# Kernel optimization log

Hardware: AMD Instinct MI355X
Metric: run time of the kernel (lower is better)

The kernel has to match this reference:

```python
import jax, jax.numpy as jnp
import numpy as np

IN_F = 256
OUT_F = 256
ALPHA = 0.01  # LeakyReLU negative slope
NEG_INF = -1e9


def setup_inputs() -> dict:
    key = jax.random.key(0)
    k_inp, k_adj, k_W, k_a = jax.random.split(key, 4)
    inp = jax.random.normal(k_inp, (8, 2048, IN_F), dtype=jnp.float32)
    adj = jax.random.randint(k_adj, (2048, 2048), 0, 2, dtype=jnp.int32)
    # xavier_uniform with gain=1.414
    gain = 1.414
    lim_W = gain * np.sqrt(6.0 / (IN_F + OUT_F))
    W = jax.random.uniform(k_W, (IN_F, OUT_F), minval=-lim_W, maxval=lim_W, dtype=jnp.float32)
    lim_a = gain * np.sqrt(6.0 / (2 * OUT_F + 1))
    a = jax.random.uniform(k_a, (2 * OUT_F, 1), minval=-lim_a, maxval=lim_a, dtype=jnp.float32)
    return {"inp": inp, "adj": adj, "W": W, "a": a}


def reference(inp, adj, W, a):
    # h: [B, N, F]
    h = jnp.matmul(inp, W)
    # Additive attention decomposed: e_ij = leaky_relu(h_i . a1 + h_j . a2)
    # (mathematically identical to concat([h_i, h_j]) @ a, without the O(N^2 * 2F) intermediate)
    a1 = a[:OUT_F, 0]  # [F]
    a2 = a[OUT_F:, 0]  # [F]
    e_src = jnp.einsum('bnf,f->bn', h, a1)  # [B, N]
    e_dst = jnp.einsum('bnf,f->bn', h, a2)  # [B, N]
    e = jax.nn.leaky_relu(e_src[:, :, None] + e_dst[:, None, :], negative_slope=ALPHA)  # [B, N, N]
    e = jnp.where(adj[None, :, :] == 0, NEG_INF, e)
    attention = jax.nn.softmax(e, axis=-1)
    # dropout is identity in eval mode
    h_prime = jnp.matmul(attention, h)  # [B, N, F]
    return jax.nn.relu(h_prime)  # concat=True path
```

## Files before the change

### kernel.cpp

```cpp
#include <hip/hip_runtime.h>
#include <hip/hip_bf16.h>
#include <stdint.h>

#define N_NODES 2048
#define FDIM 256

typedef short bf16x8 __attribute__((ext_vector_type(8)));
typedef float f32x4 __attribute__((ext_vector_type(4)));
typedef unsigned short u16x4 __attribute__((ext_vector_type(4)));

static __device__ __forceinline__ unsigned short bf16r(float x) {
  __hip_bfloat16 h = __float2bfloat16(x);
  return __builtin_bit_cast(unsigned short, h);
}

__global__ __launch_bounds__(256) void k_pp(const int* __restrict__ adj, uint32_t* __restrict__ adjp,
                                            const float* __restrict__ W, const float* __restrict__ a,
                                            __hip_bfloat16* __restrict__ WT16,
                                            float* __restrict__ wa1, float* __restrict__ wa2) {
  int bid = blockIdx.x, t = threadIdx.x;
  if (bid < 512) {
    int lane = t & 63;
    int i = bid * 4 + (t >> 6);
    const int* row = adj + (size_t)i * N_NODES;
    #pragma unroll
    for (int it = 0; it < 32; ++it) {
      int v = row[it * 64 + lane];
      unsigned long long m = __ballot(v != 0);
      if (lane == 0) {
        adjp[i * 64 + it * 2]     = (uint32_t)(m & 0xffffffffull);
        adjp[i * 64 + it * 2 + 1] = (uint32_t)(m >> 32);
      }
    }
    return;
  }
  int pb = bid - 512;
  if (pb < 16) {
    __shared__ __hip_bfloat16 T[64][67];
    int k0 = (pb & 3) * 64, f0 = (pb >> 2) * 64;
    int r = t >> 2, c0 = (t & 3) * 16;
    #pragma unroll
    for (int i = 0; i < 4; ++i) {
      f32x4 v = *(const f32x4*)(W + (size_t)(k0 + r) * FDIM + f0 + c0 + i * 4);
      #pragma unroll
      for (int j = 0; j < 4; ++j) T[r][c0 + i * 4 + j] = __float2bfloat16(v[j]);
    }
    __syncthreads();
    int fr = t >> 2, kc = (t & 3) * 16;
    unsigned short buf[16];
    #pragma unroll
    for (int i = 0; i < 16; ++i) buf[i] = __builtin_bit_cast(unsigned short, T[kc + i][fr]);
    uint4* dst = (uint4*)(WT16 + (size_t)(f0 + fr) * FDIM + k0 + kc);
    dst[0] = *(uint4*)&buf[0];
    dst[1] = *(uint4*)&buf[8];
  } else {
    int k = (pb - 16) * 64 + (t >> 2), q = t & 3;
    float s1 = 0.f, s2 = 0.f;
    #pragma unroll
    for (int i = 0; i < 16; ++i) {
      int f = q * 64 + i * 4;
      f32x4 w  = *(const f32x4*)(W + (size_t)k * FDIM + f);
      f32x4 v1 = *(const f32x4*)(a + f);
      f32x4 v2 = *(const f32x4*)(a + FDIM + f);
      #pragma unroll
      for (int j = 0; j < 4; ++j) { s1 += w[j] * v1[j]; s2 += w[j] * v2[j]; }
    }
    s1 += __shfl_xor(s1, 1); s1 += __shfl_xor(s1, 2);
    s2 += __shfl_xor(s2, 1); s2 += __shfl_xor(s2, 2);
    if (q == 0) { wa1[k] = s1; wa2[k] = s2; }
  }
}

__global__ __launch_bounds__(256) void k_h2(const float* __restrict__ inp,
                                            const __hip_bfloat16* __restrict__ WT16,
                                            const float* __restrict__ wa1, const float* __restrict__ wa2,
                                            __hip_bfloat16* __restrict__ Bf,
                                            float* __restrict__ e_src, float* __restrict__ e_dst) {
  __shared__ char lds_raw[20480];
  __hip_bfloat16* Asm = (__hip_bfloat16*)lds_raw;
  int t = threadIdx.x;
  int r0 = blockIdx.x * 32;
  int b = r0 >> 11, j0 = r0 & (N_NODES - 1);
  {
    int r = t >> 3, q = t & 7, c0 = q * 32;
    const float* ip = inp + (size_t)(r0 + r) * FDIM + c0;
    float s1 = 0.f, s2 = 0.f;
    #pragma unroll
    for (int i = 0; i < 8; ++i) {
      f32x4 v  = *(const f32x4*)(ip + i * 4);
      f32x4 u1 = *(const f32x4*)(wa1 + c0 + i * 4);
      f32x4 u2 = *(const f32x4*)(wa2 + c0 + i * 4);
      u16x4 pk;
      #pragma unroll
      for (int j = 0; j < 4; ++j) {
        s1 += v[j] * u1[j];
        s2 += v[j] * u2[j];
        pk[j] = bf16r(v[j]);
      }
      *(u16x4*)(Asm + r * 264 + c0 + i * 4) = pk;
    }
    s1 += __shfl_xor(s1, 1); s1 += __shfl_xor(s1, 2); s1 += __shfl_xor(s1, 4);
    s2 += __shfl_xor(s2, 1); s2 += __shfl_xor(s2, 2); s2 += __shfl_xor(s2, 4);
    if (q == 0) { e_src[r0 + r] = s1; e_dst[r0 + r] = s2; }
  }
  __syncthreads();

  int lane = t & 63, wv = t >> 6, l15 = lane & 15, lq = lane >> 4;
  int f0 = wv * 64;
  f32x4 acc[2][4];
  #pragma unroll
  for (int mf = 0; mf < 2; ++mf)
    #pragma unroll
    for (int nf = 0; nf < 4; ++nf)
      #pragma unroll
      for (int e = 0; e < 4; ++e) acc[mf][nf][e] = 0.f;

  #pragma unroll
  for (int ks = 0; ks < 8; ++ks) {
    int k0 = ks * 32;
    bf16x8 af[2], bfr[4];
    #pragma unroll
    for (int mf = 0; mf < 2; ++mf)
      af[mf] = *(const bf16x8*)(Asm + (mf * 16 + l15) * 264 + k0 + lq * 8);
    #pragma unroll
    for (int nf = 0; nf < 4; ++nf)
      bfr[nf] = *(const bf16x8*)(WT16 + (size_t)(f0 + nf * 16 + l15) * FDIM + k0 + lq * 8);
    #pragma unroll
    for (int mf = 0; mf < 2; ++mf)
      #pragma unroll
      for (int nf = 0; nf < 4; ++nf)
        acc[mf][nf] = __builtin_amdgcn_mfma_f32_16x16x32_bf16(af[mf], bfr[nf], acc[mf][nf], 0, 0, 0);
  }

  __syncthreads();
  __hip_bfloat16* Tsm = (__hip_bfloat16*)lds_raw;
  #pragma unroll
  for (int mf = 0; mf < 2; ++mf)
    #pragma unroll
    for (int nf = 0; nf < 4; ++nf) {
      u16x4 pk;
      #pragma unroll
      for (int r = 0; r < 4; ++r) pk[r] = bf16r(acc[mf][nf][r]);
      int fl = f0 + nf * 16 + l15;
      int jl = mf * 16 + lq * 4;
      *(u16x4*)(Tsm + fl * 40 + jl) = pk;
    }
  __syncthreads();
  {
    int kt = j0 >> 5;
    #pragma unroll
    for (int q = 0; q < 4; ++q) {
      int ft = (t >> 6) * 4 + q;
      uint4 v = *(const uint4*)(Tsm + (ft * 16 + l15) * 40 + lq * 8);
      *(uint4*)(Bf + ((((size_t)b * 16 + ft) * 64 + kt) * 64 + lane) * 8) = v;
    }
  }
}

__global__ __launch_bounds__(256) void k_ml(const uint32_t* __restrict__ adjp,
                                            const float* __restrict__ e_src,
                                            const float* __restrict__ e_dst,
                                            float* __restrict__ mrow, float* __restrict__ ilrow) {
  int t = threadIdx.x;
  int lane = t & 63;
  int r = blockIdx.x * 4 + (t >> 6);
  int b = r >> 11, i = r & (N_NODES - 1);
  float es = e_src[r];
  const float* edb = e_dst + ((size_t)b << 11);
  const uint32_t* arow = adjp + (size_t)i * 64;
  float ev[32];
  float mx = -3e38f;
  #pragma unroll
  for (int it = 0; it < 32; ++it) {
    int j = it * 64 + lane;
    float ed = edb[j];
    uint32_t w = arow[j >> 5];
    float s = es + ed;
    float lr = fmaxf(s, 0.01f * s);
    float e = ((w >> (j & 31)) & 1u) ? lr : -1e9f;
    ev[it] = e;
    mx = fmaxf(mx, e);
  }
  #pragma unroll
  for (int m = 1; m <= 32; m <<= 1) mx = fmaxf(mx, __shfl_xor(mx, m));
  float sum = 0.f;
  #pragma unroll
  for (int it = 0; it < 32; ++it) sum += __expf(ev[it] - mx);
  #pragma unroll
  for (int m = 1; m <= 32; m <<= 1) sum += __shfl_xor(sum, m);
  if (lane == 0) { mrow[r] = mx; ilrow[r] = 1.0f / sum; }
}

__global__ __launch_bounds__(512) void k_pvF3(const __hip_bfloat16* __restrict__ Bf,
                                              const uint32_t* __restrict__ adjp,
                                              const float* __restrict__ e_src,
                                              const float* __restrict__ e_dst,
                                              const float* __restrict__ mrow,
                                              const float* __restrict__ ilrow,
                                              float* __restrict__ out) {
  __shared__ __align__(16) char Abuf[32768];
  __shared__ float sm_ed[2048];
  __shared__ uint32_t sm_adj[64 * 65];
  int t = threadIdx.x;
  int b  = blockIdx.x & 7;
  int it = blockIdx.x >> 3;
  int i0 = it * 64;
  int lane = t & 63, wv = t >> 6, l15 = lane & 15, lq = lane >> 4;
  int sub = wv & 3, par = wv >> 2;

  *(f32x4*)(sm_ed + t * 4) = *(const f32x4*)(e_dst + ((size_t)b << 11) + t * 4);
  {
    int row = t >> 3, q = t & 7;
    const uint4* s = (const uint4*)(adjp + (size_t)(i0 + row) * 64 + q * 8);
    uint32_t* d = sm_adj + row * 65 + q * 8;
    uint4 v0 = s[0], v1 = s[1];
    *(uint4*)(d) = v0; *(uint4*)(d + 4) = v1;
  }
  int rg = (b << 11) + i0 + sub * 16 + l15;
  float es = e_src[rg], mi = mrow[rg], ili = ilrow[rg];
  int adjbase = (sub * 16 + l15) * 65;
  int edoff = lq * 8;
  __syncthreads();

  auto computeA = [&](int k0) -> uint4 {
    uint32_t w = sm_adj[adjbase + k0] >> (lq * 8);
    f32x4 e0 = *(const f32x4*)(sm_ed + k0 * 32 + edoff);
    f32x4 e1 = *(const f32x4*)(sm_ed + k0 * 32 + edoff + 4);
    unsigned short u[8];
    #pragma unroll
    for (int e = 0; e < 8; ++e) {
      float ed = (e < 4) ? e0[e] : e1[e - 4];
      float s = es + ed;
      float lr = fmaxf(s, 0.01f * s);
      float p = __expf(lr - mi) * ili;
      p = ((w >> e) & 1u) ? p : 0.0f;
      u[e] = bf16r(p);
    }
    uint4 v;
    v.x = (uint32_t)u[0] | ((uint32_t)u[1] << 16);
    v.y = (uint32_t)u[2] | ((uint32_t)u[3] << 16);
    v.z = (uint32_t)u[4] | ((uint32_t)u[5] << 16);
    v.w = (uint32_t)u[6] | ((uint32_t)u[7] << 16);
    return v;
  };

  auto produce = [&](int buf, int ch) {
    #pragma unroll
    for (int q = 0; q < 2; ++q) {
      int k0l = q * 2 + par;
      uint4 fr = computeA(ch * 4 + k0l);
      *(uint4*)(Abuf + (((buf * 4 + k0l) * 4 + sub) << 10) + lane * 16) = fr;
    }
  };

  const __hip_bfloat16* Bp0 = Bf + (((size_t)b * 16 + wv * 2)     * 64) * 512 + (size_t)lane * 8;
  const __hip_bfloat16* Bp1 = Bf + (((size_t)b * 16 + wv * 2 + 1) * 64) * 512 + (size_t)lane * 8;

  f32x4 acc[4][2];
  #pragma unroll
  for (int m = 0; m < 4; ++m)
    #pragma unroll
    for (int n = 0; n < 2; ++n)
      #pragma unroll
      for (int e = 0; e < 4; ++e) acc[m][n][e] = 0.f;

  bf16x8 bA0 = *(const bf16x8*)(Bp0);
  bf16x8 bA1 = *(const bf16x8*)(Bp1);
  bf16x8 bB0 = *(const bf16x8*)(Bp0 + 512);
  bf16x8 bB1 = *(const bf16x8*)(Bp1 + 512);

  produce(0, 0);
  __syncthreads();

  for (int ch = 0; ch < 16; ++ch) {
    int buf = ch & 1;
    if (ch < 15) produce(buf ^ 1, ch + 1);
    const char* Ab = Abuf + buf * 16384;
    #pragma unroll
    for (int k0l = 0; k0l < 4; ++k0l) {
      int k0 = ch * 4 + k0l;
      bf16x8 af[4];
      #pragma unroll
      for (int m = 0; m < 4; ++m)
        af[m] = *(const bf16x8*)(Ab + ((k0l * 4 + m) << 10) + lane * 16);
      bf16x8 cb0 = (k0l & 1) ? bB0 : bA0;
      bf16x8 cb1 = (k0l & 1) ? bB1 : bA1;
      if (k0 + 2 < 64) {
        if (k0l & 1) { bB0 = *(const bf16x8*)(Bp0 + (size_t)(k0 + 2) * 512); bB1 = *(const bf16x8*)(Bp1 + (size_t)(k0 + 2) * 512); }
        else         { bA0 = *(const bf16x8*)(Bp0 + (size_t)(k0 + 2) * 512); bA1 = *(const bf16x8*)(Bp1 + (size_t)(k0 + 2) * 512); }
      }
      #pragma unroll
      for (int m = 0; m < 4; ++m) {
        acc[m][0] = __builtin_amdgcn_mfma_f32_16x16x32_bf16(af[m], cb0, acc[m][0], 0, 0, 0);
        acc[m][1] = __builtin_amdgcn_mfma_f32_16x16x32_bf16(af[m], cb1, acc[m][1], 0, 0, 0);
      }
    }
    __syncthreads();
  }

  #pragma unroll
  for (int m = 0; m < 4; ++m)
    #pragma unroll
    for (int n = 0; n < 2; ++n) {
      int col = (wv * 2 + n) * 16 + l15;
      int orow = (b << 11) + i0 + m * 16 + lq * 4;
      #pragma unroll
      for (int r = 0; r < 4; ++r)
        out[(size_t)(orow + r) * FDIM + col] = fmaxf(acc[m][n][r], 0.0f);
    }
}

extern "C" void kernel_launch(void* const* d_in, const int* in_sizes, int n_in,
                              void* d_out, int out_size, void* d_ws, size_t ws_size,
                              hipStream_t stream) {
  const float* inp = (const float*)d_in[0];
  const int*   adj = (const int*)d_in[1];
  const float* W   = (const float*)d_in[2];
  const float* a   = (const float*)d_in[3];
  float* out = (float*)d_out;
  char* ws = (char*)d_ws;

  __hip_bfloat16* Bf   = (__hip_bfloat16*)ws;
  float* e_src         = (float*)(ws + 8388608);
  float* e_dst         = (float*)(ws + 8454144);
  float* mrow          = (float*)(ws + 8519680);
  float* ilrow         = (float*)(ws + 8585216);
  __hip_bfloat16* WT16 = (__hip_bfloat16*)(ws + 8650752);
  float* wa1           = (float*)(ws + 8781824);
  float* wa2           = (float*)(ws + 8782848);
  uint32_t* adjp       = (uint32_t*)(ws + 8783872);

  k_pp<<<532, 256, 0, stream>>>(adj, adjp, W, a, WT16, wa1, wa2);
  k_h2<<<512, 256, 0, stream>>>(inp, WT16, wa1, wa2, Bf, e_src, e_dst);
  k_ml<<<4096, 256, 0, stream>>>(adjp, e_src, e_dst, mrow, ilrow);
  k_pvF3<<<256, 512, 0, stream>>>(Bf, adjp, e_src, e_dst, mrow, ilrow, out);
}
```

Baseline: 81.11 us.

## Fuse softmax row stats into PV kernel and adj packing into h kernel

Drops the separate row max/sum kernel. Each PV block now computes the softmax max and inverse sum for its 64 rows from the e_dst and adjacency data already in LDS, then keeps them in shared memory. The adjacency bit-packing also moves out of the prep kernel into the h-projection kernel, which cuts the launch count from four to three. In exchange each PV block repeats the softmax-statistics pass before its main loop, adding a serial prologue and more register pressure to a kernel that runs only 256 blocks.

```diff
diff --git a/kernel.cpp b/kernel.cpp
--- a/kernel.cpp
+++ b/kernel.cpp
@@ -14,30 +14,13 @@
   return __builtin_bit_cast(unsigned short, h);
 }
 
-__global__ __launch_bounds__(256) void k_pp(const int* __restrict__ adj, uint32_t* __restrict__ adjp,
-                                            const float* __restrict__ W, const float* __restrict__ a,
-                                            __hip_bfloat16* __restrict__ WT16,
-                                            float* __restrict__ wa1, float* __restrict__ wa2) {
+__global__ __launch_bounds__(256) void k_prep(const float* __restrict__ W, const float* __restrict__ a,
+                                              __hip_bfloat16* __restrict__ WT16,
+                                              float* __restrict__ wa1, float* __restrict__ wa2) {
   int bid = blockIdx.x, t = threadIdx.x;
-  if (bid < 512) {
-    int lane = t & 63;
-    int i = bid * 4 + (t >> 6);
-    const int* row = adj + (size_t)i * N_NODES;
-    #pragma unroll
-    for (int it = 0; it < 32; ++it) {
-      int v = row[it * 64 + lane];
-      unsigned long long m = __ballot(v != 0);
-      if (lane == 0) {
-        adjp[i * 64 + it * 2]     = (uint32_t)(m & 0xffffffffull);
-        adjp[i * 64 + it * 2 + 1] = (uint32_t)(m >> 32);
-      }
-    }
-    return;
-  }
-  int pb = bid - 512;
-  if (pb < 16) {
+  if (bid < 16) {
     __shared__ __hip_bfloat16 T[64][67];
-    int k0 = (pb & 3) * 64, f0 = (pb >> 2) * 64;
+    int k0 = (bid & 3) * 64, f0 = (bid >> 2) * 64;
     int r = t >> 2, c0 = (t & 3) * 16;
     #pragma unroll
     for (int i = 0; i < 4; ++i) {
@@ -54,7 +37,7 @@
     dst[0] = *(uint4*)&buf[0];
     dst[1] = *(uint4*)&buf[8];
   } else {
-    int k = (pb - 16) * 64 + (t >> 2), q = t & 3;
+    int k = (bid - 16) * 64 + (t >> 2), q = t & 3;
     float s1 = 0.f, s2 = 0.f;
     #pragma unroll
     for (int i = 0; i < 16; ++i) {
@@ -71,16 +54,33 @@
   }
 }
 
-__global__ __launch_bounds__(256) void k_h2(const float* __restrict__ inp,
-                                            const __hip_bfloat16* __restrict__ WT16,
-                                            const float* __restrict__ wa1, const float* __restrict__ wa2,
-                                            __hip_bfloat16* __restrict__ Bf,
-                                            float* __restrict__ e_src, float* __restrict__ e_dst) {
+__global__ __launch_bounds__(256) void k_h2p(const float* __restrict__ inp,
+                                             const int* __restrict__ adj, uint32_t* __restrict__ adjp,
+                                             const __hip_bfloat16* __restrict__ WT16,
+                                             const float* __restrict__ wa1, const float* __restrict__ wa2,
+                                             __hip_bfloat16* __restrict__ Bf,
+                                             float* __restrict__ e_src, float* __restrict__ e_dst) {
   __shared__ char lds_raw[20480];
   __hip_bfloat16* Asm = (__hip_bfloat16*)lds_raw;
   int t = threadIdx.x;
   int r0 = blockIdx.x * 32;
   int b = r0 >> 11, j0 = r0 & (N_NODES - 1);
+
+  {
+    int prow = blockIdx.x * 4 + (t >> 6);
+    int lane = t & 63;
+    const int* row = adj + (size_t)prow * N_NODES;
+    #pragma unroll
+    for (int it = 0; it < 32; ++it) {
+      int v = row[it * 64 + lane];
+      unsigned long long m = __ballot(v != 0);
+      if (lane == 0) {
+        adjp[prow * 64 + it * 2]     = (uint32_t)(m & 0xffffffffull);
+        adjp[prow * 64 + it * 2 + 1] = (uint32_t)(m >> 32);
+      }
+    }
+  }
+
   {
     int r = t >> 3, q = t & 7, c0 = q * 32;
     const float* ip = inp + (size_t)(r0 + r) * FDIM + c0;
@@ -157,50 +157,15 @@
   }
 }
 
-__global__ __launch_bounds__(256) void k_ml(const uint32_t* __restrict__ adjp,
-                                            const float* __restrict__ e_src,
-                                            const float* __restrict__ e_dst,
-                                            float* __restrict__ mrow, float* __restrict__ ilrow) {
-  int t = threadIdx.x;
-  int lane = t & 63;
-  int r = blockIdx.x * 4 + (t >> 6);
-  int b = r >> 11, i = r & (N_NODES - 1);
-  float es = e_src[r];
-  const float* edb = e_dst + ((size_t)b << 11);
-  const uint32_t* arow = adjp + (size_t)i * 64;
-  float ev[32];
-  float mx = -3e38f;
-  #pragma unroll
-  for (int it = 0; it < 32; ++it) {
-    int j = it * 64 + lane;
-    float ed = edb[j];
-    uint32_t w = arow[j >> 5];
-    float s = es + ed;
-    float lr = fmaxf(s, 0.01f * s);
-    float e = ((w >> (j & 31)) & 1u) ? lr : -1e9f;
-    ev[it] = e;
-    mx = fmaxf(mx, e);
-  }
-  #pragma unroll
-  for (int m = 1; m <= 32; m <<= 1) mx = fmaxf(mx, __shfl_xor(mx, m));
-  float sum = 0.f;
-  #pragma unroll
-  for (int it = 0; it < 32; ++it) sum += __expf(ev[it] - mx);
-  #pragma unroll
-  for (int m = 1; m <= 32; m <<= 1) sum += __shfl_xor(sum, m);
-  if (lane == 0) { mrow[r] = mx; ilrow[r] = 1.0f / sum; }
-}
-
-__global__ __launch_bounds__(512) void k_pvF3(const __hip_bfloat16* __restrict__ Bf,
+__global__ __launch_bounds__(512) void k_pvF4(const __hip_bfloat16* __restrict__ Bf,
                                               const uint32_t* __restrict__ adjp,
                                               const float* __restrict__ e_src,
                                               const float* __restrict__ e_dst,
-                                              const float* __restrict__ mrow,
-                                              const float* __restrict__ ilrow,
                                               float* __restrict__ out) {
   __shared__ __align__(16) char Abuf[32768];
   __shared__ float sm_ed[2048];
   __shared__ uint32_t sm_adj[64 * 65];
+  __shared__ float sm_es[64], sm_m[64], sm_il[64];
   int t = threadIdx.x;
   int b  = blockIdx.x & 7;
   int it = blockIdx.x >> 3;
@@ -216,11 +181,38 @@
     uint4 v0 = s[0], v1 = s[1];
     *(uint4*)(d) = v0; *(uint4*)(d + 4) = v1;
   }
-  int rg = (b << 11) + i0 + sub * 16 + l15;
-  float es = e_src[rg], mi = mrow[rg], ili = ilrow[rg];
-  int adjbase = (sub * 16 + l15) * 65;
+  __syncthreads();
+
+  for (int rr = 0; rr < 8; ++rr) {
+    int iloc = wv * 8 + rr;
+    float es = e_src[(b << 11) + i0 + iloc];
+    float ev[32];
+    float mx = -3e38f;
+    #pragma unroll
+    for (int c = 0; c < 32; ++c) {
+      int j = c * 64 + lane;
+      float s = es + sm_ed[j];
+      float lr = fmaxf(s, 0.01f * s);
+      uint32_t w = sm_adj[iloc * 65 + (j >> 5)];
+      float e = ((w >> (j & 31)) & 1u) ? lr : -1e9f;
+      ev[c] = e;
+      mx = fmaxf(mx, e);
+    }
+    #pragma unroll
+    for (int m = 1; m <= 32; m <<= 1) mx = fmaxf(mx, __shfl_xor(mx, m));
+    float sum = 0.f;
+    #pragma unroll
+    for (int c = 0; c < 32; ++c) sum += __expf(ev[c] - mx);
+    #pragma unroll
+    for (int m = 1; m <= 32; m <<= 1) sum += __shfl_xor(sum, m);
+    if (lane == 0) { sm_es[iloc] = es; sm_m[iloc] = mx; sm_il[iloc] = 1.0f / sum; }
+  }
+  __syncthreads();
+
+  int fr_row = sub * 16 + l15;
+  float es = sm_es[fr_row], mi = sm_m[fr_row], ili = sm_il[fr_row];
+  int adjbase = fr_row * 65;
   int edoff = lq * 8;
-  __syncthreads();
 
   auto computeA = [&](int k0) -> uint4 {
     uint32_t w = sm_adj[adjbase + k0] >> (lq * 8);
@@ -323,15 +315,12 @@
   __hip_bfloat16* Bf   = (__hip_bfloat16*)ws;
   float* e_src         = (float*)(ws + 8388608);
   float* e_dst         = (float*)(ws + 8454144);
-  float* mrow          = (float*)(ws + 8519680);
-  float* ilrow         = (float*)(ws + 8585216);
-  __hip_bfloat16* WT16 = (__hip_bfloat16*)(ws + 8650752);
-  float* wa1           = (float*)(ws + 8781824);
-  float* wa2           = (float*)(ws + 8782848);
-  uint32_t* adjp       = (uint32_t*)(ws + 8783872);
-
-  k_pp<<<532, 256, 0, stream>>>(adj, adjp, W, a, WT16, wa1, wa2);
-  k_h2<<<512, 256, 0, stream>>>(inp, WT16, wa1, wa2, Bf, e_src, e_dst);
-  k_ml<<<4096, 256, 0, stream>>>(adjp, e_src, e_dst, mrow, ilrow);
-  k_pvF3<<<256, 512, 0, stream>>>(Bf, adjp, e_src, e_dst, mrow, ilrow, out);
-}
+  __hip_bfloat16* WT16 = (__hip_bfloat16*)(ws + 8519680);
+  float* wa1           = (float*)(ws + 8650752);
+  float* wa2           = (float*)(ws + 8651776);
+  uint32_t* adjp       = (uint32_t*)(ws + 8652800);
+
+  k_prep<<<20, 256, 0, stream>>>(W, a, WT16, wa1, wa2);
+  k_h2p<<<512, 256, 0, stream>>>(inp, adj, adjp, WT16, wa1, wa2, Bf, e_src, e_dst);
+  k_pvF4<<<256, 512, 0, stream>>>(Bf, adjp, e_src, e_dst, out);
+}
```

Result: no change. 81.99 us (+1.1%).

## Split PV kernel across feature halves and fuse adjacency packing into projection

Applied to the files above, without the earlier changes.

The attention-times-V kernel now processes 32 rows and half of the feature columns per 256-thread block, launching 1024 blocks instead of 256 blocks of 512 threads. This gives more blocks for the GPU's compute units and cuts LDS use per block. The cost is that each block recomputes the softmax probabilities for its rows, so that work is done twice. Adjacency bit-packing moves from the prep kernel into the projection kernel, so the prep kernel shrinks to a 20-block launch.

```diff
diff --git a/kernel.cpp b/kernel.cpp
--- a/kernel.cpp
+++ b/kernel.cpp
@@ -14,30 +14,13 @@
   return __builtin_bit_cast(unsigned short, h);
 }
 
-__global__ __launch_bounds__(256) void k_pp(const int* __restrict__ adj, uint32_t* __restrict__ adjp,
-                                            const float* __restrict__ W, const float* __restrict__ a,
-                                            __hip_bfloat16* __restrict__ WT16,
-                                            float* __restrict__ wa1, float* __restrict__ wa2) {
+__global__ __launch_bounds__(256) void k_prep(const float* __restrict__ W, const float* __restrict__ a,
+                                              __hip_bfloat16* __restrict__ WT16,
+                                              float* __restrict__ wa1, float* __restrict__ wa2) {
   int bid = blockIdx.x, t = threadIdx.x;
-  if (bid < 512) {
-    int lane = t & 63;
-    int i = bid * 4 + (t >> 6);
-    const int* row = adj + (size_t)i * N_NODES;
-    #pragma unroll
-    for (int it = 0; it < 32; ++it) {
-      int v = row[it * 64 + lane];
-      unsigned long long m = __ballot(v != 0);
-      if (lane == 0) {
-        adjp[i * 64 + it * 2]     = (uint32_t)(m & 0xffffffffull);
-        adjp[i * 64 + it * 2 + 1] = (uint32_t)(m >> 32);
-      }
-    }
-    return;
-  }
-  int pb = bid - 512;
-  if (pb < 16) {
+  if (bid < 16) {
     __shared__ __hip_bfloat16 T[64][67];
-    int k0 = (pb & 3) * 64, f0 = (pb >> 2) * 64;
+    int k0 = (bid & 3) * 64, f0 = (bid >> 2) * 64;
     int r = t >> 2, c0 = (t & 3) * 16;
     #pragma unroll
     for (int i = 0; i < 4; ++i) {
@@ -54,7 +37,7 @@
     dst[0] = *(uint4*)&buf[0];
     dst[1] = *(uint4*)&buf[8];
   } else {
-    int k = (pb - 16) * 64 + (t >> 2), q = t & 3;
+    int k = (bid - 16) * 64 + (t >> 2), q = t & 3;
     float s1 = 0.f, s2 = 0.f;
     #pragma unroll
     for (int i = 0; i < 16; ++i) {
@@ -71,16 +54,33 @@
   }
 }
 
-__global__ __launch_bounds__(256) void k_h2(const float* __restrict__ inp,
-                                            const __hip_bfloat16* __restrict__ WT16,
-                                            const float* __restrict__ wa1, const float* __restrict__ wa2,
-                                            __hip_bfloat16* __restrict__ Bf,
-                                            float* __restrict__ e_src, float* __restrict__ e_dst) {
+__global__ __launch_bounds__(256) void k_h2p(const float* __restrict__ inp,
+                                             const int* __restrict__ adj, uint32_t* __restrict__ adjp,
+                                             const __hip_bfloat16* __restrict__ WT16,
+                                             const float* __restrict__ wa1, const float* __restrict__ wa2,
+                                             __hip_bfloat16* __restrict__ Bf,
+                                             float* __restrict__ e_src, float* __restrict__ e_dst) {
   __shared__ char lds_raw[20480];
   __hip_bfloat16* Asm = (__hip_bfloat16*)lds_raw;
   int t = threadIdx.x;
   int r0 = blockIdx.x * 32;
   int b = r0 >> 11, j0 = r0 & (N_NODES - 1);
+
+  {
+    int prow = blockIdx.x * 4 + (t >> 6);
+    int lane = t & 63;
+    const int* row = adj + (size_t)prow * N_NODES;
+    #pragma unroll
+    for (int it = 0; it < 32; ++it) {
+      int v = row[it * 64 + lane];
+      unsigned long long m = __ballot(v != 0);
+      if (lane == 0) {
+        adjp[prow * 64 + it * 2]     = (uint32_t)(m & 0xffffffffull);
+        adjp[prow * 64 + it * 2 + 1] = (uint32_t)(m >> 32);
+      }
+    }
+  }
+
   {
     int r = t >> 3, q = t & 7, c0 = q * 32;
     const float* ip = inp + (size_t)(r0 + r) * FDIM + c0;
@@ -191,24 +191,30 @@
   if (lane == 0) { mrow[r] = mx; ilrow[r] = 1.0f / sum; }
 }
 
-__global__ __launch_bounds__(512) void k_pvF3(const __hip_bfloat16* __restrict__ Bf,
+__global__ __launch_bounds__(256) void k_pvF5(const __hip_bfloat16* __restrict__ Bf,
                                               const uint32_t* __restrict__ adjp,
                                               const float* __restrict__ e_src,
                                               const float* __restrict__ e_dst,
                                               const float* __restrict__ mrow,
                                               const float* __restrict__ ilrow,
                                               float* __restrict__ out) {
-  __shared__ __align__(16) char Abuf[32768];
+  __shared__ __align__(16) char Abuf[16384];
   __shared__ float sm_ed[2048];
-  __shared__ uint32_t sm_adj[64 * 65];
+  __shared__ uint32_t sm_adj[32 * 65];
   int t = threadIdx.x;
   int b  = blockIdx.x & 7;
-  int it = blockIdx.x >> 3;
-  int i0 = it * 64;
+  int it = (blockIdx.x >> 3) & 63;
+  int fh = blockIdx.x >> 9;
+  int i0 = it * 32;
   int lane = t & 63, wv = t >> 6, l15 = lane & 15, lq = lane >> 4;
-  int sub = wv & 3, par = wv >> 2;
-
-  *(f32x4*)(sm_ed + t * 4) = *(const f32x4*)(e_dst + ((size_t)b << 11) + t * 4);
+  int sub = wv & 1, par = wv >> 1;
+
+  {
+    f32x4 v0 = *(const f32x4*)(e_dst + ((size_t)b << 11) + t * 8);
+    f32x4 v1 = *(const f32x4*)(e_dst + ((size_t)b << 11) + t * 8 + 4);
+    *(f32x4*)(sm_ed + t * 8) = v0;
+    *(f32x4*)(sm_ed + t * 8 + 4) = v1;
+  }
   {
     int row = t >> 3, q = t & 7;
     const uint4* s = (const uint4*)(adjp + (size_t)(i0 + row) * 64 + q * 8);
@@ -216,9 +222,10 @@
     uint4 v0 = s[0], v1 = s[1];
     *(uint4*)(d) = v0; *(uint4*)(d + 4) = v1;
   }
-  int rg = (b << 11) + i0 + sub * 16 + l15;
+  int fr_row = sub * 16 + l15;
+  int rg = (b << 11) + i0 + fr_row;
   float es = e_src[rg], mi = mrow[rg], ili = ilrow[rg];
-  int adjbase = (sub * 16 + l15) * 65;
+  int adjbase = fr_row * 65;
   int edoff = lq * 8;
   __syncthreads();
 
@@ -249,16 +256,16 @@
     for (int q = 0; q < 2; ++q) {
       int k0l = q * 2 + par;
       uint4 fr = computeA(ch * 4 + k0l);
-      *(uint4*)(Abuf + (((buf * 4 + k0l) * 4 + sub) << 10) + lane * 16) = fr;
+      *(uint4*)(Abuf + (((buf * 4 + k0l) * 2 + sub) << 10) + lane * 16) = fr;
     }
   };
 
-  const __hip_bfloat16* Bp0 = Bf + (((size_t)b * 16 + wv * 2)     * 64) * 512 + (size_t)lane * 8;
-  const __hip_bfloat16* Bp1 = Bf + (((size_t)b * 16 + wv * 2 + 1) * 64) * 512 + (size_t)lane * 8;
-
-  f32x4 acc[4][2];
-  #pragma unroll
-  for (int m = 0; m < 4; ++m)
+  const __hip_bfloat16* Bp0 = Bf + (((size_t)b * 16 + fh * 8 + wv * 2)     * 64) * 512 + (size_t)lane * 8;
+  const __hip_bfloat16* Bp1 = Bf + (((size_t)b * 16 + fh * 8 + wv * 2 + 1) * 64) * 512 + (size_t)lane * 8;
+
+  f32x4 acc[2][2];
+  #pragma unroll
+  for (int m = 0; m < 2; ++m)
     #pragma unroll
     for (int n = 0; n < 2; ++n)
       #pragma unroll
@@ -275,14 +282,14 @@
   for (int ch = 0; ch < 16; ++ch) {
     int buf = ch & 1;
     if (ch < 15) produce(buf ^ 1, ch + 1);
-    const char* Ab = Abuf + buf * 16384;
+    const char* Ab = Abuf + buf * 8192;
     #pragma unroll
     for (int k0l = 0; k0l < 4; ++k0l) {
       int k0 = ch * 4 + k0l;
-      bf16x8 af[4];
-      #pragma unroll
-      for (int m = 0; m < 4; ++m)
-        af[m] = *(const bf16x8*)(Ab + ((k0l * 4 + m) << 10) + lane * 16);
+      bf16x8 af[2];
+      #pragma unroll
+      for (int m = 0; m < 2; ++m)
+        af[m] = *(const bf16x8*)(Ab + ((k0l * 2 + m) << 10) + lane * 16);
       bf16x8 cb0 = (k0l & 1) ? bB0 : bA0;
       bf16x8 cb1 = (k0l & 1) ? bB1 : bA1;
       if (k0 + 2 < 64) {
@@ -290,7 +297,7 @@
         else         { bA0 = *(const bf16x8*)(Bp0 + (size_t)(k0 + 2) * 512); bA1 = *(const bf16x8*)(Bp1 + (size_t)(k0 + 2) * 512); }
       }
       #pragma unroll
-      for (int m = 0; m < 4; ++m) {
+      for (int m = 0; m < 2; ++m) {
         acc[m][0] = __builtin_amdgcn_mfma_f32_16x16x32_bf16(af[m], cb0, acc[m][0], 0, 0, 0);
         acc[m][1] = __builtin_amdgcn_mfma_f32_16x16x32_bf16(af[m], cb1, acc[m][1], 0, 0, 0);
       }
@@ -299,10 +306,10 @@
   }
 
   #pragma unroll
-  for (int m = 0; m < 4; ++m)
+  for (int m = 0; m < 2; ++m)
     #pragma unroll
     for (int n = 0; n < 2; ++n) {
-      int col = (wv * 2 + n) * 16 + l15;
+      int col = (fh * 8 + wv * 2 + n) * 16 + l15;
       int orow = (b << 11) + i0 + m * 16 + lq * 4;
       #pragma unroll
       for (int r = 0; r < 4; ++r)
@@ -330,8 +337,8 @@
   float* wa2           = (float*)(ws + 8782848);
   uint32_t* adjp       = (uint32_t*)(ws + 8783872);
 
-  k_pp<<<532, 256, 0, stream>>>(adj, adjp, W, a, WT16, wa1, wa2);
-  k_h2<<<512, 256, 0, stream>>>(inp, WT16, wa1, wa2, Bf, e_src, e_dst);
+  k_prep<<<20, 256, 0, stream>>>(W, a, WT16, wa1, wa2);
+  k_h2p<<<512, 256, 0, stream>>>(inp, adj, adjp, WT16, wa1, wa2, Bf, e_src, e_dst);
   k_ml<<<4096, 256, 0, stream>>>(adjp, e_src, e_dst, mrow, ilrow);
-  k_pvF3<<<256, 512, 0, stream>>>(Bf, adjp, e_src, e_dst, mrow, ilrow, out);
-}
+  k_pvF5<<<1024, 256, 0, stream>>>(Bf, adjp, e_src, e_dst, mrow, ilrow, out);
+}
```

Measured after the change: 87.13 us. +7.4%, slower.
